# Kernel tuning notes

Measured on AMD Instinct MI355X. Metric: run time of the kernel, lower is better.

Reference implementation:

```python
import jax, jax.numpy as jnp
import numpy as np

B, S, H = 1, 2048, 4608
NH, NKV, HD = 36, 4, 128
GROUP = NH // NKV  # 9
ROPE_THETA = 100000.0
SLIDING_WINDOW = 1024


def _rope_tables(seq_len, head_dim):
    inv_freq = 1.0 / (ROPE_THETA ** (jnp.arange(0, head_dim, 2, dtype=jnp.float32) / head_dim))
    ang = jnp.arange(seq_len, dtype=jnp.float32)[:, None] * inv_freq[None, :]  # [S, HD/2]
    emb = jnp.concatenate([ang, ang], axis=-1)  # [S, HD]
    return jnp.cos(emb), jnp.sin(emb)


def setup_inputs() -> dict:
    key = jax.random.key(0)
    ks = jax.random.split(key, 10)
    std = 0.02
    cos_table, sin_table = _rope_tables(S, HD)
    return {
        "hidden_states": jax.random.normal(ks[0], (B, S, H), jnp.float32),
        "position_ids": jnp.broadcast_to(jnp.arange(S, dtype=jnp.int64)[None, :], (B, S)),
        "cos_table": cos_table,
        "sin_table": sin_table,
        "q_w": jax.random.normal(ks[1], (NH * HD, H), jnp.float32) * std,
        "q_b": jax.random.normal(ks[2], (NH * HD,), jnp.float32) * std,
        "k_w": jax.random.normal(ks[3], (NKV * HD, H), jnp.float32) * std,
        "k_b": jax.random.normal(ks[4], (NKV * HD,), jnp.float32) * std,
        "v_w": jax.random.normal(ks[5], (NKV * HD, H), jnp.float32) * std,
        "v_b": jax.random.normal(ks[6], (NKV * HD,), jnp.float32) * std,
        "o_w": jax.random.normal(ks[7], (H, NH * HD), jnp.float32) * std,
        "o_b": jax.random.normal(ks[8], (H,), jnp.float32) * std,
        "sliding_window": SLIDING_WINDOW,
    }


def _rotate_half(x):
    x1, x2 = jnp.split(x, 2, axis=-1)
    return jnp.concatenate([-x2, x1], axis=-1)


def reference(hidden_states, position_ids, cos_table, sin_table,
              q_w, q_b, k_w, k_b, v_w, v_b, o_w, o_b, sliding_window):
    bsz, q_len, _ = hidden_states.shape
    scaling = HD ** -0.5

    q = (hidden_states @ q_w.T + q_b).reshape(bsz, q_len, NH, HD)
    k = (hidden_states @ k_w.T + k_b).reshape(bsz, q_len, NKV, HD)
    v = (hidden_states @ v_w.T + v_b).reshape(bsz, q_len, NKV, HD)

    # RoPE with explicit cos/sin, unsqueeze_dim=2 ('bsnd' layout)
    cos = cos_table[position_ids][:, :, None, :]  # [B, S, 1, HD]
    sin = sin_table[position_ids][:, :, None, :]
    q = q * cos + _rotate_half(q) * sin
    k = k * cos + _rotate_half(k) * sin

    # GQA: group Q heads per KV head
    qg = q.reshape(bsz, q_len, NKV, GROUP, HD)
    logits = jnp.einsum('bqgrd,bkgd->bgrqk', qg, k) * scaling  # [B, NKV, GROUP, S, S]

    # causal + sliding-window mask: attend where k <= q and q - k < window
    idx = jnp.arange(q_len)
    mask = (idx[:, None] >= idx[None, :]) & (idx[:, None] - idx[None, :] < sliding_window)
    logits = jnp.where(mask[None, None, None, :, :], logits, jnp.finfo(logits.dtype).min)

    probs = jax.nn.softmax(logits, axis=-1)
    attn = jnp.einsum('bgrqk,bkgd->bqgrd', probs, v).reshape(bsz, q_len, NH * HD)
    return attn @ o_w.T + o_b
```

## Files before the change

kernel.cpp:

```cpp
#include <hip/hip_runtime.h>
#include <stdint.h>

typedef __attribute__((ext_vector_type(8))) __bf16 bf16x8;
typedef __attribute__((ext_vector_type(4))) float f32x4;
typedef __attribute__((ext_vector_type(8))) unsigned short u16x8;
typedef __attribute__((ext_vector_type(4))) unsigned short u16x4;

#define SEQ 2048
#define HID 4608
#define NQKV 5632
#define NHEAD 36
#define NKVH 4
#define HDIM 128
#define WINDOW 1024

__device__ __forceinline__ unsigned short f2b(float f) {
    unsigned u = __builtin_bit_cast(unsigned, f);
    u += 0x7fffu + ((u >> 16) & 1u);
    return (unsigned short)(u >> 16);
}
__device__ __forceinline__ float b2f(unsigned short h) {
    unsigned u = ((unsigned)h) << 16;
    return __builtin_bit_cast(float, u);
}

#define GLD16(gp, lp) __builtin_amdgcn_global_load_lds( \
    (const __attribute__((address_space(1))) void*)(gp), \
    (__attribute__((address_space(3))) void*)(lp), 16, 0, 0)

#define VMCNT8() asm volatile("s_waitcnt vmcnt(8)" ::: "memory")
#define VMCNT5() asm volatile("s_waitcnt vmcnt(5)" ::: "memory")
#define VMCNT4() asm volatile("s_waitcnt vmcnt(4)" ::: "memory")
#define VMCNT0() asm volatile("s_waitcnt vmcnt(0)" ::: "memory")
#define BARRIER() asm volatile("s_barrier" ::: "memory")

__global__ __launch_bounds__(256) void conv_all_kernel(
    const float* __restrict__ s0, unsigned short* __restrict__ d0, int n0,
    const float* __restrict__ s1, unsigned short* __restrict__ d1, int n1,
    const float* __restrict__ s2, unsigned short* __restrict__ d2, int n2,
    const float* __restrict__ s3, unsigned short* __restrict__ d3, int n3)
{
    int total = n0 + n1 + n2 + n3;
    int stride = gridDim.x * blockDim.x;
    for (int i = blockIdx.x * blockDim.x + threadIdx.x; i < total; i += stride) {
        const float* src; unsigned short* dst; int j = i;
        if (j < n0) { src = s0; dst = d0; }
        else if ((j -= n0) < n1) { src = s1; dst = d1; }
        else if ((j -= n1) < n2) { src = s2; dst = d2; }
        else { j -= n2; src = s3; dst = d3; }
        float4 v = ((const float4*)src)[j];
        ushort4 o;
        o.x = f2b(v.x); o.y = f2b(v.y); o.z = f2b(v.z); o.w = f2b(v.w);
        ((ushort4*)dst)[j] = o;
    }
}

__global__ __launch_bounds__(512, 2) void gemm256_kernel(
    const unsigned short* __restrict__ A,
    const unsigned short* __restrict__ W,
    void* __restrict__ out,
    const float* __restrict__ b0, const float* __restrict__ b1, const float* __restrict__ b2,
    int N, int K, int GX, int GB, int outf32,
    const float* __restrict__ cw_src, unsigned short* __restrict__ cw_dst, int cw_n4)
{
    const int tid = threadIdx.x;
    const int o = blockIdx.x;

    if (o >= GB) {
        int cb = o - GB, ncb = gridDim.x - GB;
        int stride = ncb * 512;
        for (int i = cb * 512 + tid; i < cw_n4; i += stride) {
            float4 v = ((const float4*)cw_src)[i];
            ushort4 u;
            u.x = f2b(v.x); u.y = f2b(v.y); u.z = f2b(v.z); u.w = f2b(v.w);
            ((ushort4*)cw_dst)[i] = u;
        }
        return;
    }

    __shared__ alignas(16) unsigned short ldsA[2][256 * 64];
    __shared__ alignas(16) unsigned short ldsB[2][256 * 64];

    const int w = tid >> 6, lane = tid & 63;
    const int r16 = lane & 15, kg = lane >> 4;
    const int wm = w >> 2, wn = w & 3;

    const int cpx = GB >> 3;
    const int id = (o & 7) * cpx + (o >> 3);
    const int bx = id % GX, by = id / GX;
    const int row0 = by * 256, col0 = bx * 256;

    const int lr = lane >> 3;
    const int lc = lane & 7;
    const int cg = lc ^ lr;
    const unsigned short* Abase = A + (size_t)row0 * K;
    const unsigned short* Wbase = W + (size_t)col0 * K;

    auto STG = [&](const unsigned short* Mat, unsigned short* ldsSlot, int hf, int kb) {
#pragma unroll
        for (int j = 0; j < 2; ++j) {
            int row = hf * 128 + (w * 2 + j) * 8 + lr;
            GLD16(Mat + (size_t)row * K + kb + cg * 8,
                  (char*)ldsSlot + hf * 16384 + (w * 2 + j) * 1024);
        }
    };

    const int NITER = K >> 7;
    f32x4 acc[8][4] = {};
    const int swz = r16 & 7;

    bf16x8 af[4][2], bfA[2][2], bfB[2][2];

#define DSR_A(mh, Sl) \
_Pragma("unroll") for (int mi = 0; mi < 4; ++mi) \
_Pragma("unroll") for (int kh = 0; kh < 2; ++kh) \
    af[mi][kh] = *(const bf16x8*)((Sl) + (wm * 128 + (mh) * 64 + mi * 16 + r16) * 64 + ((kh * 4 + kg) ^ swz) * 8);
#define DSR_B(nh, Sl, BF) \
_Pragma("unroll") for (int ni = 0; ni < 2; ++ni) \
_Pragma("unroll") for (int kh = 0; kh < 2; ++kh) \
    BF[ni][kh] = *(const bf16x8*)((Sl) + (wn * 64 + (nh) * 32 + ni * 16 + r16) * 64 + ((kh * 4 + kg) ^ swz) * 8);
#define MFMA_Q(mh, nh, BF) \
    asm volatile("s_waitcnt lgkmcnt(0)" ::: "memory"); \
    __builtin_amdgcn_sched_barrier(0); \
    __builtin_amdgcn_s_setprio(1); \
_Pragma("unroll") for (int mi = 0; mi < 4; ++mi) \
_Pragma("unroll") for (int ni = 0; ni < 2; ++ni) \
_Pragma("unroll") for (int kh = 0; kh < 2; ++kh) \
    acc[(mh) * 4 + mi][(nh) * 2 + ni] = __builtin_amdgcn_mfma_f32_16x16x32_bf16(af[mi][kh], BF[ni][kh], acc[(mh) * 4 + mi][(nh) * 2 + ni], 0, 0, 0); \
    __builtin_amdgcn_s_setprio(0); \
    __builtin_amdgcn_sched_barrier(0);

    STG(Abase, ldsA[0], 0, 0);  STG(Abase, ldsA[0], 1, 0);
    STG(Wbase, ldsB[0], 0, 0);  STG(Wbase, ldsB[0], 1, 0);
    STG(Abase, ldsA[1], 0, 64); STG(Abase, ldsA[1], 1, 64);
    STG(Wbase, ldsB[1], 0, 64); STG(Wbase, ldsB[1], 1, 64);
    VMCNT0();
    BARRIER();

    for (int i = 0; i < NITER; ++i) {
        const unsigned short* A0 = ldsA[0];
        const unsigned short* B0 = ldsB[0];
        const unsigned short* A1 = ldsA[1];
        const unsigned short* B1 = ldsB[1];
        const bool st = (i + 1 < NITER);
        const int kb0 = (i + 1) * 128;
        const int kb1 = kb0 + 64;

        DSR_A(0, A0); DSR_B(0, B0, bfA);
        BARRIER();
        MFMA_Q(0, 0, bfA);
        BARRIER();
        DSR_B(1, B0, bfB);
        BARRIER();
        MFMA_Q(0, 1, bfB);
        BARRIER();
        DSR_A(1, A0);
        if (st) STG(Wbase, ldsB[0], 0, kb0);
        BARRIER();
        MFMA_Q(1, 1, bfB);
        BARRIER();
        if (st) { STG(Abase, ldsA[0], 0, kb0); VMCNT4(); } else { VMCNT0(); }
        BARRIER();
        MFMA_Q(1, 0, bfA);
        BARRIER();
        DSR_A(0, A1); DSR_B(0, B1, bfA);
        if (st) STG(Abase, ldsA[0], 1, kb0);
        BARRIER();
        MFMA_Q(0, 0, bfA);
        BARRIER();
        DSR_B(1, B1, bfB);
        if (st) STG(Wbase, ldsB[0], 1, kb0);
        BARRIER();
        MFMA_Q(0, 1, bfB);
        BARRIER();
        DSR_A(1, A1);
        if (st) { STG(Wbase, ldsB[1], 0, kb1); STG(Wbase, ldsB[1], 1, kb1); }
        BARRIER();
        MFMA_Q(1, 1, bfB);
        BARRIER();
        if (st) { STG(Abase, ldsA[1], 0, kb1); STG(Abase, ldsA[1], 1, kb1); VMCNT8(); }
        BARRIER();
        MFMA_Q(1, 0, bfA);
        BARRIER();
    }

    if (!outf32) {
        unsigned short* O = (unsigned short*)out;
#pragma unroll
        for (int m = 0; m < 8; ++m)
#pragma unroll
            for (int n = 0; n < 4; ++n)
#pragma unroll
                for (int r = 0; r < 4; ++r) {
                    int row = row0 + wm * 128 + m * 16 + kg * 4 + r;
                    int col = col0 + wn * 64 + n * 16 + r16;
                    float bias = (col < HID) ? b0[col]
                               : (col < HID + 512 ? b1[col - HID] : b2[col - HID - 512]);
                    O[(size_t)row * N + col] = f2b(acc[m][n][r] + bias);
                }
    } else {
        float* O = (float*)out;
#pragma unroll
        for (int m = 0; m < 8; ++m)
#pragma unroll
            for (int n = 0; n < 4; ++n)
#pragma unroll
                for (int r = 0; r < 4; ++r) {
                    int row = row0 + wm * 128 + m * 16 + kg * 4 + r;
                    int col = col0 + wn * 64 + n * 16 + r16;
                    O[(size_t)row * N + col] = acc[m][n][r] + b0[col];
                }
    }
#undef DSR_A
#undef DSR_B
#undef MFMA_Q
}

__global__ __launch_bounds__(512, 4) void gemm_op_kernel(
    const unsigned short* __restrict__ A,
    const unsigned short* __restrict__ W,
    float* __restrict__ out,
    const float* __restrict__ b0,
    int N, int K, int GX)
{
    __shared__ alignas(16) unsigned short ldsA[2][128 * 64];
    __shared__ alignas(16) unsigned short ldsB[2][192 * 64];

    const int tid = threadIdx.x;
    const int w = tid >> 6, lane = tid & 63;
    const int r16 = lane & 15, kg = lane >> 4;
    const int wm = w >> 2, wn = w & 3;

    const int cpx = gridDim.x >> 3;
    const int o = blockIdx.x;
    const int id = (o & 7) * cpx + (o >> 3);
    const int bx = id % GX, by = id / GX;
    const int row0 = by * 128, col0 = bx * 192;

    const int lr = lane >> 3;
    const int lc = lane & 7;
    const int cg = lc ^ lr;
    const unsigned short* Abase = A + (size_t)row0 * K;
    const unsigned short* Wbase = W + (size_t)col0 * K;

    auto STGA = [&](unsigned short* slot, int kb) {
#pragma unroll
        for (int j = 0; j < 2; ++j) {
            int row = (w * 2 + j) * 8 + lr;
            GLD16(Abase + (size_t)row * K + kb + cg * 8,
                  (char*)slot + (w * 2 + j) * 1024);
        }
    };
    auto STGB = [&](unsigned short* slot, int kb) {
#pragma unroll
        for (int j3 = 0; j3 < 3; ++j3) {
            int row = j3 * 64 + w * 8 + lr;
            GLD16(Wbase + (size_t)row * K + kb + cg * 8,
                  (char*)slot + j3 * 8192 + w * 1024);
        }
    };

    const int NITER = K >> 7;
    f32x4 acc[4][3] = {};
    const int swz = r16 & 7;

    bf16x8 af[4][2], bf[3][2];

#define DSR_AF(Sl) \
_Pragma("unroll") for (int mi = 0; mi < 4; ++mi) \
_Pragma("unroll") for (int kh = 0; kh < 2; ++kh) \
    af[mi][kh] = *(const bf16x8*)((Sl) + (wm * 64 + mi * 16 + r16) * 64 + ((kh * 4 + kg) ^ swz) * 8);
#define DSR_BF(Sl) \
_Pragma("unroll") for (int ni = 0; ni < 3; ++ni) \
_Pragma("unroll") for (int kh = 0; kh < 2; ++kh) \
    bf[ni][kh] = *(const bf16x8*)((Sl) + (wn * 48 + ni * 16 + r16) * 64 + ((kh * 4 + kg) ^ swz) * 8);
#define MFMA12(half) \
    asm volatile("s_waitcnt lgkmcnt(0)" ::: "memory"); \
    __builtin_amdgcn_sched_barrier(0); \
    __builtin_amdgcn_s_setprio(1); \
_Pragma("unroll") for (int mi = 0; mi < 2; ++mi) \
_Pragma("unroll") for (int ni = 0; ni < 3; ++ni) \
_Pragma("unroll") for (int kh = 0; kh < 2; ++kh) \
    acc[(half) * 2 + mi][ni] = __builtin_amdgcn_mfma_f32_16x16x32_bf16(af[(half) * 2 + mi][kh], bf[ni][kh], acc[(half) * 2 + mi][ni], 0, 0, 0); \
    __builtin_amdgcn_s_setprio(0); \
    __builtin_amdgcn_sched_barrier(0);

    STGA(ldsA[0], 0);  STGB(ldsB[0], 0);
    STGA(ldsA[1], 64); STGB(ldsB[1], 64);
    VMCNT0();
    BARRIER();

    for (int i = 0; i < NITER; ++i) {
        const bool st = (i + 1 < NITER);
        const int kb0 = (i + 1) * 128;
        const int kb1 = kb0 + 64;

        DSR_AF(ldsA[0]); DSR_BF(ldsB[0]);
        BARRIER();
        MFMA12(0);
        BARRIER();
        if (st) { STGA(ldsA[0], kb0); STGB(ldsB[0], kb0); VMCNT5(); } else { VMCNT0(); }
        BARRIER();
        MFMA12(1);
        BARRIER();
        DSR_AF(ldsA[1]); DSR_BF(ldsB[1]);
        BARRIER();
        MFMA12(0);
        BARRIER();
        if (st) { STGA(ldsA[1], kb1); STGB(ldsB[1], kb1); VMCNT5(); }
        BARRIER();
        MFMA12(1);
        BARRIER();
    }

#pragma unroll
    for (int m = 0; m < 4; ++m)
#pragma unroll
        for (int n = 0; n < 3; ++n)
#pragma unroll
            for (int r = 0; r < 4; ++r) {
                int row = row0 + wm * 64 + m * 16 + kg * 4 + r;
                int col = col0 + wn * 48 + n * 16 + r16;
                out[(size_t)row * N + col] = acc[m][n][r] + b0[col];
            }
#undef DSR_AF
#undef DSR_BF
#undef MFMA12
}

__global__ __launch_bounds__(256) void rope_vt_kernel(unsigned short* __restrict__ qkv,
                                                      const float* __restrict__ cos_t,
                                                      const float* __restrict__ sin_t,
                                                      unsigned short* __restrict__ vtg) {
    const int bid = blockIdx.x;
    if (bid < 5120) {
        int idx = bid * 256 + threadIdx.x;
        int d4 = idx & 15;
        int t2 = idx >> 4;
        int head = t2 % 40;
        int s = t2 / 40;
        int base = head < NHEAD ? head * HDIM : HID + (head - NHEAD) * HDIM;
        size_t off = (size_t)s * NQKV + base + d4 * 4;
        u16x4 xv = *(const u16x4*)(qkv + off);
        u16x4 yv = *(const u16x4*)(qkv + off + 64);
        float4 c = *(const float4*)(cos_t + s * HDIM + d4 * 4);
        float4 sn = *(const float4*)(sin_t + s * HDIM + d4 * 4);
        u16x4 xo, yo;
        float x, y;
        x = b2f(xv[0]); y = b2f(yv[0]); xo[0] = f2b(x * c.x - y * sn.x); yo[0] = f2b(y * c.x + x * sn.x);
        x = b2f(xv[1]); y = b2f(yv[1]); xo[1] = f2b(x * c.y - y * sn.y); yo[1] = f2b(y * c.y + x * sn.y);
        x = b2f(xv[2]); y = b2f(yv[2]); xo[2] = f2b(x * c.z - y * sn.z); yo[2] = f2b(y * c.z + x * sn.z);
        x = b2f(xv[3]); y = b2f(yv[3]); xo[3] = f2b(x * c.w - y * sn.w); yo[3] = f2b(y * c.w + x * sn.w);
        *(u16x4*)(qkv + off) = xo;
        *(u16x4*)(qkv + off + 64) = yo;
    } else {
        __shared__ unsigned short tile[32][36];
        int vb = bid - 5120;
        const int s0 = (vb & 63) * 32;
        const int d0 = ((vb >> 6) & 3) * 32;
        const int kvh = vb >> 8;
        const int lid = threadIdx.x;
        {
            int sl = lid >> 3, dc = (lid & 7) * 4;
            u16x4 v = *(const u16x4*)(qkv + (size_t)(s0 + sl) * NQKV + HID + 512 + kvh * HDIM + d0 + dc);
#pragma unroll
            for (int i = 0; i < 4; ++i) tile[sl][dc + i] = v[i];
        }
        __syncthreads();
        {
            int dl = lid >> 3, sc = (lid & 7) * 4;
            u16x4 v;
#pragma unroll
            for (int i = 0; i < 4; ++i) v[i] = tile[sc + i][dl];
            *(u16x4*)(vtg + (size_t)kvh * HDIM * SEQ + (size_t)(d0 + dl) * SEQ + s0 + sc) = v;
        }
    }
}

#define KSTR 136
#define VSTR 72
#define PSTR 88
__global__ __launch_bounds__(256) void attn_kernel(const unsigned short* __restrict__ qkv,
                                                   const unsigned short* __restrict__ vtg,
                                                   unsigned short* __restrict__ aout)
{
    __shared__ alignas(16) unsigned short Ks[64 * KSTR];
    __shared__ alignas(16) unsigned short Vt[128 * VSTR];
    __shared__ alignas(16) unsigned short Ps[4 * 16 * PSTR];
    const int h = blockIdx.x, qb = blockIdx.y;
    const int q0 = qb * 64;
    const int kvh = h / 9;
    const int tid = threadIdx.x, wid = tid >> 6, lane = tid & 63;
    const int r16 = lane & 15, kg = lane >> 4;
    const int qbase = q0 + wid * 16;
    const unsigned short* vsrc = vtg + (size_t)kvh * HDIM * SEQ;

    bf16x8 qf[4];
    {
        const unsigned short* qrow = qkv + (size_t)(qbase + r16) * NQKV + h * HDIM;
#pragma unroll
        for (int kk = 0; kk < 4; ++kk)
            qf[kk] = *(const bf16x8*)(qrow + kk * 32 + kg * 8);
    }

    f32x4 o[8] = {};
    float mrow[4], lrow[4];
#pragma unroll
    for (int r = 0; r < 4; ++r) { mrow[r] = -1e30f; lrow[r] = 0.f; }

    int lo = q0 - (WINDOW - 1); if (lo < 0) lo = 0; lo &= ~63;
    unsigned short* myP = Ps + wid * 16 * PSTR;
    const float scale = 0.08838834764831845f;

    u16x8 kreg[4], vreg[4];
#define PREF(KT) \
_Pragma("unroll") for (int j = 0; j < 4; ++j) { \
        int c = tid + j * 256; \
        int key = c >> 4, dc = c & 15; \
        kreg[j] = *(const u16x8*)(qkv + (size_t)((KT) + key) * NQKV + HID + kvh * HDIM + dc * 8); \
        int d = c >> 3, k8 = (c & 7) * 8; \
        vreg[j] = *(const u16x8*)(vsrc + (size_t)d * SEQ + (KT) + k8); \
    }

    PREF(lo);

    for (int kt = lo; kt <= q0; kt += 64) {
#pragma unroll
        for (int j = 0; j < 4; ++j) {
            int c = tid + j * 256;
            int key = c >> 4, dc = c & 15;
            *(u16x8*)(Ks + key * KSTR + dc * 8) = kreg[j];
            int d = c >> 3, k8 = (c & 7) * 8;
            *(u16x8*)(Vt + d * VSTR + k8) = vreg[j];
        }
        __syncthreads();

        if (kt + 64 <= q0) { PREF(kt + 64); }

        f32x4 sc[4] = {};
#pragma unroll
        for (int t = 0; t < 4; ++t)
#pragma unroll
            for (int kk = 0; kk < 4; ++kk) {
                bf16x8 kf = *(const bf16x8*)(Ks + (t * 16 + r16) * KSTR + kk * 32 + kg * 8);
                sc[t] = __builtin_amdgcn_mfma_f32_16x16x32_bf16(qf[kk], kf, sc[t], 0, 0, 0);
            }

        float p[4][4], mt[4];
#pragma unroll
        for (int r = 0; r < 4; ++r) mt[r] = -1e30f;
        const bool fullv = (kt + 63 <= qbase) && (qbase + 15 - kt < WINDOW);
        if (fullv) {
#pragma unroll
            for (int t = 0; t < 4; ++t)
#pragma unroll
                for (int r = 0; r < 4; ++r) {
                    float v = sc[t][r] * scale;
                    p[t][r] = v;
                    mt[r] = fmaxf(mt[r], v);
                }
        } else {
#pragma unroll
            for (int t = 0; t < 4; ++t)
#pragma unroll
                for (int r = 0; r < 4; ++r) {
                    int q = qbase + kg * 4 + r;
                    int key = kt + t * 16 + r16;
                    bool valid = (key <= q) && (q - key < WINDOW);
                    float v = valid ? sc[t][r] * scale : -1e30f;
                    p[t][r] = v;
                    mt[r] = fmaxf(mt[r], v);
                }
        }
#pragma unroll
        for (int mask = 1; mask <= 8; mask <<= 1)
#pragma unroll
            for (int r = 0; r < 4; ++r)
                mt[r] = fmaxf(mt[r], __shfl_xor(mt[r], mask, 64));

        float alpha[4], tsum[4];
#pragma unroll
        for (int r = 0; r < 4; ++r) {
            float mnew = fmaxf(mrow[r], mt[r]);
            alpha[r] = __expf(mrow[r] - mnew);
            mrow[r] = mnew;
            tsum[r] = 0.f;
        }
#pragma unroll
        for (int t = 0; t < 4; ++t)
#pragma unroll
            for (int r = 0; r < 4; ++r) {
                float e = __expf(p[t][r] - mrow[r]);
                p[t][r] = e;
                tsum[r] += e;
            }
#pragma unroll
        for (int mask = 1; mask <= 8; mask <<= 1)
#pragma unroll
            for (int r = 0; r < 4; ++r)
                tsum[r] += __shfl_xor(tsum[r], mask, 64);
#pragma unroll
        for (int r = 0; r < 4; ++r)
            lrow[r] = lrow[r] * alpha[r] + tsum[r];
#pragma unroll
        for (int n = 0; n < 8; ++n)
#pragma unroll
            for (int r = 0; r < 4; ++r)
                o[n][r] = o[n][r] * alpha[r];

#pragma unroll
        for (int t = 0; t < 4; ++t)
#pragma unroll
            for (int r = 0; r < 4; ++r)
                myP[(kg * 4 + r) * PSTR + t * 16 + r16] = f2b(p[t][r]);
        asm volatile("s_waitcnt lgkmcnt(0)" ::: "memory");

#pragma unroll
        for (int kc = 0; kc < 2; ++kc) {
            bf16x8 pa = *(const bf16x8*)(myP + r16 * PSTR + kc * 32 + kg * 8);
#pragma unroll
            for (int n = 0; n < 8; ++n) {
                bf16x8 vb = *(const bf16x8*)(Vt + (n * 16 + r16) * VSTR + kc * 32 + kg * 8);
                o[n] = __builtin_amdgcn_mfma_f32_16x16x32_bf16(pa, vb, o[n], 0, 0, 0);
            }
        }
        BARRIER();
    }
#undef PREF

#pragma unroll
    for (int n = 0; n < 8; ++n)
#pragma unroll
        for (int r = 0; r < 4; ++r) {
            int q = qbase + kg * 4 + r;
            aout[(size_t)q * HID + h * HDIM + n * 16 + r16] = f2b(o[n][r] / lrow[r]);
        }
}

extern "C" void kernel_launch(void* const* d_in, const int* in_sizes, int n_in,
                              void* d_out, int out_size, void* d_ws, size_t ws_size,
                              hipStream_t stream) {
    const float* hidden = (const float*)d_in[0];
    const float* cos_t = (const float*)d_in[2];
    const float* sin_t = (const float*)d_in[3];
    const float* q_w = (const float*)d_in[4];
    const float* q_b = (const float*)d_in[5];
    const float* k_w = (const float*)d_in[6];
    const float* k_b = (const float*)d_in[7];
    const float* v_w = (const float*)d_in[8];
    const float* v_b = (const float*)d_in[9];
    const float* o_w = (const float*)d_in[10];
    const float* o_b = (const float*)d_in[11];

    char* ws = (char*)d_ws;
    unsigned short* hbf  = (unsigned short*)ws;
    unsigned short* attn = hbf;
    unsigned short* wqkv = (unsigned short*)(ws + 18874368);
    unsigned short* vtg  = wqkv;
    unsigned short* wo   = (unsigned short*)(ws + 70778880);
    unsigned short* qkv  = (unsigned short*)(ws + 113246208);

    dim3 blk(256);
    conv_all_kernel<<<4096, blk, 0, stream>>>(
        hidden, hbf,                          (SEQ * HID) / 4,
        q_w,    wqkv,                         (HID * HID) / 4,
        k_w,    wqkv + (size_t)HID * HID,     (512 * HID) / 4,
        v_w,    wqkv + (size_t)5120 * HID,    (512 * HID) / 4);

    gemm256_kernel<<<dim3(256), dim3(512), 0, stream>>>(
        hbf, wqkv, qkv, q_b, k_b, v_b, NQKV, HID, 22, 176, 0,
        o_w, wo, (HID * HID) / 4);
    rope_vt_kernel<<<6144, blk, 0, stream>>>(qkv, cos_t, sin_t, vtg);
    attn_kernel<<<dim3(NHEAD, SEQ / 64), blk, 0, stream>>>(qkv, vtg, attn);
    gemm_op_kernel<<<dim3(384), dim3(512), 0, stream>>>(
        attn, wo, (float*)d_out, o_b, HID, HID, 24);
}
```

Baseline: 364.2 us.

## Shrink QKV GEMM tile to 128x128 for more blocks and occupancy

Replaces the 256x256 QKV projection tile with a 128x128 tile and raises launch bounds to 4 blocks per SM. This gives 704 GEMM blocks plus 128 o_w conversion blocks instead of 176 plus 80. The aim is to fix poor wave quantization (176 tiles on 256 CUs) and raise occupancy. The cost is lower arithmetic intensity per tile, more global/L2 traffic for the A and W operands, and a simpler pipeline schedule. It also drops the unused f32 output path.

```diff
diff --git a/kernel.cpp b/kernel.cpp
--- a/kernel.cpp
+++ b/kernel.cpp
@@ -28,7 +28,6 @@
     (const __attribute__((address_space(1))) void*)(gp), \
     (__attribute__((address_space(3))) void*)(lp), 16, 0, 0)
 
-#define VMCNT8() asm volatile("s_waitcnt vmcnt(8)" ::: "memory")
 #define VMCNT5() asm volatile("s_waitcnt vmcnt(5)" ::: "memory")
 #define VMCNT4() asm volatile("s_waitcnt vmcnt(4)" ::: "memory")
 #define VMCNT0() asm volatile("s_waitcnt vmcnt(0)" ::: "memory")
@@ -55,12 +54,12 @@
     }
 }
 
-__global__ __launch_bounds__(512, 2) void gemm256_kernel(
+__global__ __launch_bounds__(512, 4) void gemm_qkv_kernel(
     const unsigned short* __restrict__ A,
     const unsigned short* __restrict__ W,
-    void* __restrict__ out,
+    unsigned short* __restrict__ out,
     const float* __restrict__ b0, const float* __restrict__ b1, const float* __restrict__ b2,
-    int N, int K, int GX, int GB, int outf32,
+    int N, int K, int GX, int GB,
     const float* __restrict__ cw_src, unsigned short* __restrict__ cw_dst, int cw_n4)
 {
     const int tid = threadIdx.x;
@@ -78,8 +77,8 @@
         return;
     }
 
-    __shared__ alignas(16) unsigned short ldsA[2][256 * 64];
-    __shared__ alignas(16) unsigned short ldsB[2][256 * 64];
+    __shared__ alignas(16) unsigned short ldsA[2][128 * 64];
+    __shared__ alignas(16) unsigned short ldsB[2][128 * 64];
 
     const int w = tid >> 6, lane = tid & 63;
     const int r16 = lane & 15, kg = lane >> 4;
@@ -88,7 +87,7 @@
     const int cpx = GB >> 3;
     const int id = (o & 7) * cpx + (o >> 3);
     const int bx = id % GX, by = id / GX;
-    const int row0 = by * 256, col0 = bx * 256;
+    const int row0 = by * 128, col0 = bx * 128;
 
     const int lr = lane >> 3;
     const int lc = lane & 7;
@@ -96,124 +95,83 @@
     const unsigned short* Abase = A + (size_t)row0 * K;
     const unsigned short* Wbase = W + (size_t)col0 * K;
 
-    auto STG = [&](const unsigned short* Mat, unsigned short* ldsSlot, int hf, int kb) {
+    auto STG = [&](const unsigned short* Mat, unsigned short* slot, int kb) {
 #pragma unroll
         for (int j = 0; j < 2; ++j) {
-            int row = hf * 128 + (w * 2 + j) * 8 + lr;
+            int row = (w * 2 + j) * 8 + lr;
             GLD16(Mat + (size_t)row * K + kb + cg * 8,
-                  (char*)ldsSlot + hf * 16384 + (w * 2 + j) * 1024);
+                  (char*)slot + (w * 2 + j) * 1024);
         }
     };
 
     const int NITER = K >> 7;
-    f32x4 acc[8][4] = {};
+    f32x4 acc[4][2] = {};
     const int swz = r16 & 7;
 
-    bf16x8 af[4][2], bfA[2][2], bfB[2][2];
-
-#define DSR_A(mh, Sl) \
+    bf16x8 af[4][2], bf[2][2];
+
+#define DSR_AF(Sl) \
 _Pragma("unroll") for (int mi = 0; mi < 4; ++mi) \
 _Pragma("unroll") for (int kh = 0; kh < 2; ++kh) \
-    af[mi][kh] = *(const bf16x8*)((Sl) + (wm * 128 + (mh) * 64 + mi * 16 + r16) * 64 + ((kh * 4 + kg) ^ swz) * 8);
-#define DSR_B(nh, Sl, BF) \
+    af[mi][kh] = *(const bf16x8*)((Sl) + (wm * 64 + mi * 16 + r16) * 64 + ((kh * 4 + kg) ^ swz) * 8);
+#define DSR_BF(Sl) \
 _Pragma("unroll") for (int ni = 0; ni < 2; ++ni) \
 _Pragma("unroll") for (int kh = 0; kh < 2; ++kh) \
-    BF[ni][kh] = *(const bf16x8*)((Sl) + (wn * 64 + (nh) * 32 + ni * 16 + r16) * 64 + ((kh * 4 + kg) ^ swz) * 8);
-#define MFMA_Q(mh, nh, BF) \
+    bf[ni][kh] = *(const bf16x8*)((Sl) + (wn * 32 + ni * 16 + r16) * 64 + ((kh * 4 + kg) ^ swz) * 8);
+#define MFMA8(half) \
     asm volatile("s_waitcnt lgkmcnt(0)" ::: "memory"); \
     __builtin_amdgcn_sched_barrier(0); \
     __builtin_amdgcn_s_setprio(1); \
-_Pragma("unroll") for (int mi = 0; mi < 4; ++mi) \
+_Pragma("unroll") for (int mi = 0; mi < 2; ++mi) \
 _Pragma("unroll") for (int ni = 0; ni < 2; ++ni) \
 _Pragma("unroll") for (int kh = 0; kh < 2; ++kh) \
-    acc[(mh) * 4 + mi][(nh) * 2 + ni] = __builtin_amdgcn_mfma_f32_16x16x32_bf16(af[mi][kh], BF[ni][kh], acc[(mh) * 4 + mi][(nh) * 2 + ni], 0, 0, 0); \
+    acc[(half) * 2 + mi][ni] = __builtin_amdgcn_mfma_f32_16x16x32_bf16(af[(half) * 2 + mi][kh], bf[ni][kh], acc[(half) * 2 + mi][ni], 0, 0, 0); \
     __builtin_amdgcn_s_setprio(0); \
     __builtin_amdgcn_sched_barrier(0);
 
-    STG(Abase, ldsA[0], 0, 0);  STG(Abase, ldsA[0], 1, 0);
-    STG(Wbase, ldsB[0], 0, 0);  STG(Wbase, ldsB[0], 1, 0);
-    STG(Abase, ldsA[1], 0, 64); STG(Abase, ldsA[1], 1, 64);
-    STG(Wbase, ldsB[1], 0, 64); STG(Wbase, ldsB[1], 1, 64);
+    STG(Abase, ldsA[0], 0);  STG(Wbase, ldsB[0], 0);
+    STG(Abase, ldsA[1], 64); STG(Wbase, ldsB[1], 64);
     VMCNT0();
     BARRIER();
 
     for (int i = 0; i < NITER; ++i) {
-        const unsigned short* A0 = ldsA[0];
-        const unsigned short* B0 = ldsB[0];
-        const unsigned short* A1 = ldsA[1];
-        const unsigned short* B1 = ldsB[1];
         const bool st = (i + 1 < NITER);
         const int kb0 = (i + 1) * 128;
         const int kb1 = kb0 + 64;
 
-        DSR_A(0, A0); DSR_B(0, B0, bfA);
-        BARRIER();
-        MFMA_Q(0, 0, bfA);
-        BARRIER();
-        DSR_B(1, B0, bfB);
-        BARRIER();
-        MFMA_Q(0, 1, bfB);
-        BARRIER();
-        DSR_A(1, A0);
-        if (st) STG(Wbase, ldsB[0], 0, kb0);
-        BARRIER();
-        MFMA_Q(1, 1, bfB);
-        BARRIER();
-        if (st) { STG(Abase, ldsA[0], 0, kb0); VMCNT4(); } else { VMCNT0(); }
-        BARRIER();
-        MFMA_Q(1, 0, bfA);
-        BARRIER();
-        DSR_A(0, A1); DSR_B(0, B1, bfA);
-        if (st) STG(Abase, ldsA[0], 1, kb0);
-        BARRIER();
-        MFMA_Q(0, 0, bfA);
-        BARRIER();
-        DSR_B(1, B1, bfB);
-        if (st) STG(Wbase, ldsB[0], 1, kb0);
-        BARRIER();
-        MFMA_Q(0, 1, bfB);
-        BARRIER();
-        DSR_A(1, A1);
-        if (st) { STG(Wbase, ldsB[1], 0, kb1); STG(Wbase, ldsB[1], 1, kb1); }
-        BARRIER();
-        MFMA_Q(1, 1, bfB);
-        BARRIER();
-        if (st) { STG(Abase, ldsA[1], 0, kb1); STG(Abase, ldsA[1], 1, kb1); VMCNT8(); }
-        BARRIER();
-        MFMA_Q(1, 0, bfA);
-        BARRIER();
-    }
-
-    if (!outf32) {
-        unsigned short* O = (unsigned short*)out;
-#pragma unroll
-        for (int m = 0; m < 8; ++m)
-#pragma unroll
-            for (int n = 0; n < 4; ++n)
-#pragma unroll
-                for (int r = 0; r < 4; ++r) {
-                    int row = row0 + wm * 128 + m * 16 + kg * 4 + r;
-                    int col = col0 + wn * 64 + n * 16 + r16;
-                    float bias = (col < HID) ? b0[col]
-                               : (col < HID + 512 ? b1[col - HID] : b2[col - HID - 512]);
-                    O[(size_t)row * N + col] = f2b(acc[m][n][r] + bias);
-                }
-    } else {
-        float* O = (float*)out;
-#pragma unroll
-        for (int m = 0; m < 8; ++m)
-#pragma unroll
-            for (int n = 0; n < 4; ++n)
-#pragma unroll
-                for (int r = 0; r < 4; ++r) {
-                    int row = row0 + wm * 128 + m * 16 + kg * 4 + r;
-                    int col = col0 + wn * 64 + n * 16 + r16;
-                    O[(size_t)row * N + col] = acc[m][n][r] + b0[col];
-                }
-    }
-#undef DSR_A
-#undef DSR_B
-#undef MFMA_Q
+        DSR_AF(ldsA[0]); DSR_BF(ldsB[0]);
+        BARRIER();
+        MFMA8(0);
+        BARRIER();
+        if (st) { STG(Abase, ldsA[0], kb0); STG(Wbase, ldsB[0], kb0); VMCNT4(); } else { VMCNT0(); }
+        BARRIER();
+        MFMA8(1);
+        BARRIER();
+        DSR_AF(ldsA[1]); DSR_BF(ldsB[1]);
+        BARRIER();
+        MFMA8(0);
+        BARRIER();
+        if (st) { STG(Abase, ldsA[1], kb1); STG(Wbase, ldsB[1], kb1); VMCNT4(); }
+        BARRIER();
+        MFMA8(1);
+        BARRIER();
+    }
+
+#pragma unroll
+    for (int m = 0; m < 4; ++m)
+#pragma unroll
+        for (int n = 0; n < 2; ++n)
+#pragma unroll
+            for (int r = 0; r < 4; ++r) {
+                int row = row0 + wm * 64 + m * 16 + kg * 4 + r;
+                int col = col0 + wn * 32 + n * 16 + r16;
+                float bias = (col < HID) ? b0[col]
+                           : (col < HID + 512 ? b1[col - HID] : b2[col - HID - 512]);
+                out[(size_t)row * N + col] = f2b(acc[m][n][r] + bias);
+            }
+#undef DSR_AF
+#undef DSR_BF
+#undef MFMA8
 }
 
 __global__ __launch_bounds__(512, 4) void gemm_op_kernel(
@@ -567,8 +525,8 @@
         k_w,    wqkv + (size_t)HID * HID,     (512 * HID) / 4,
         v_w,    wqkv + (size_t)5120 * HID,    (512 * HID) / 4);
 
-    gemm256_kernel<<<dim3(256), dim3(512), 0, stream>>>(
-        hbf, wqkv, qkv, q_b, k_b, v_b, NQKV, HID, 22, 176, 0,
+    gemm_qkv_kernel<<<dim3(832), dim3(512), 0, stream>>>(
+        hbf, wqkv, qkv, q_b, k_b, v_b, NQKV, HID, 44, 704,
         o_w, wo, (HID * HID) / 4);
     rope_vt_kernel<<<6144, blk, 0, stream>>>(qkv, cos_t, sin_t, vtg);
     attn_kernel<<<dim3(NHEAD, SEQ / 64), blk, 0, stream>>>(qkv, vtg, attn);
```

After: 381.7 us. 1.05x slower.
